# Kernel tuning notes

Measured on AMD Instinct MI355X. Metric: run time of the kernel, lower is better.

The kernel has to match this reference:

```python
import jax, jax.numpy as jnp
import numpy as np

B, NA, NB, DIM = 1024, 48, 24, 680  # batch, res_alpha(=res_gamma), res_beta, irreps dim = sum_{l<=7}(2l+1)^2


def setup_inputs() -> dict:
    key = jax.random.key(0)
    k1, k2, k3 = jax.random.split(key, 3)
    features = jax.random.normal(k1, (B, DIM), dtype=jnp.float32)
    D = jax.random.normal(k2, (NA, NB, NA, DIM), dtype=jnp.float32)  # stands in for the precomputed Wigner-D buffer
    qw = jax.random.uniform(k3, (NB,), dtype=jnp.float32)  # quadrature weights over beta
    return {"features": features, "D": D, "qw": qw}


def reference(features, D, qw):
    dim = D.shape[-1]
    scale = float(np.sqrt(dim))
    # to_grid: '...i,abci->...abc' / sqrt(dim)
    grid = jnp.einsum('ni,abci->nabc', features, D) / scale  # (B, na, nb, na)
    # from_grid: '...abc,abci,b->...i' * sqrt(dim)  (qw contracts the beta axis)
    out = jnp.einsum('nabc,abci,b->ni', grid, D, qw) * scale  # (B, dim)
    return out
```

## Files before the change

kernel.cpp:

```cpp
#include <hip/hip_runtime.h>
#include <stdint.h>

#define DIM    680
#define DPAD   768
#define NB_Q   24
#define SPLITS 72
#define STAGES 12
#define NTILE  6

typedef __bf16 bf16x8 __attribute__((ext_vector_type(8)));
typedef __bf16 bf16x2 __attribute__((ext_vector_type(2)));
typedef float  f32x16 __attribute__((ext_vector_type(16)));

typedef __attribute__((address_space(3))) unsigned       lds_u32;
typedef __attribute__((address_space(1))) const unsigned glb_u32;

__constant__ int c_tj[NTILE] = {0, 0, 0, 1, 1, 2};
__constant__ int c_ti[NTILE] = {0, 1, 2, 1, 2, 2};

static __device__ __forceinline__ unsigned f2bf(float x) {
    union { float f; unsigned u; } c; c.f = x;
    unsigned u = c.u;
    return (u + 0x7FFFu + ((u >> 16) & 1u)) >> 16;
}

static __device__ __forceinline__ unsigned pk2(float lo, float hi) {
    bf16x2 v = {(__bf16)lo, (__bf16)hi};
    return __builtin_bit_cast(unsigned, v);
}

static __device__ __forceinline__ float bf2f(unsigned short h) {
    union { unsigned u; float f; } c; c.u = ((unsigned)h) << 16;
    return c.f;
}

__global__ __launch_bounds__(512) void k12_gram(
        const float* __restrict__ D, const float* __restrict__ qw,
        uint2* __restrict__ parts) {
    __shared__ float sq[NB_Q];
    __shared__ uint4 smA[2048];
    __shared__ uint4 smB[2048];
    const int t  = threadIdx.x;
    const int h       = blockIdx.x;
    const int logical = (h & 7) * 54 + (h >> 3);
    const int split   = logical / 6;
    const int t6      = logical % 6;
    const int tj    = c_tj[t6];
    const int ti    = c_ti[t6];
    const bool diag = (tj == ti);
    const int cl_ = t & 255;
    const int hg  = t >> 8;
    const int cA  = tj * 256 + cl_;
    const int cB  = ti * 256 + cl_;
    const bool vA = (cA < DIM);
    const bool vB = (cB < DIM);
    const int cAc = vA ? cA : (DIM - 1);
    const int cBc = vB ? cB : (DIM - 1);
    const int wave  = t >> 6;
    const int lane  = t & 63;
    const int wm    = wave & 3;
    const int wn    = wave >> 2;
    const int cl    = lane & 31;
    const int half  = lane >> 5;

    f32x16 acc[2][4];
    const f32x16 zero = {};
#pragma unroll
    for (int a = 0; a < 2; ++a)
#pragma unroll
        for (int b = 0; b < 4; ++b) acc[a][b] = zero;

    float ra[32], rb[32];

#define K12_LOAD(reg_, st_, csrc_)                                            \
    do {                                                                      \
        const int g0_ = (split * STAGES + (st_)) * 64 + hg * 32;              \
        _Pragma("unroll")                                                     \
        for (int u_ = 0; u_ < 32; ++u_)                                       \
            reg_[u_] = D[(size_t)(g0_ + u_) * DIM + (csrc_)];                 \
    } while (0)

#define K12_CONV(reg_, valid_, sm_, st_)                                      \
    do {                                                                      \
        const int gg_ = (split * STAGES + (st_)) * 64 + hg * 32;              \
        _Pragma("unroll")                                                     \
        for (int kcg_ = 0; kcg_ < 4; ++kcg_) {                                \
            const int G_ = gg_ + kcg_ * 8;                                    \
            const int q_ = G_ / 48;                                           \
            const int r_ = G_ - q_ * 48;                                      \
            const float s0_ = sq[q_ % 24];                                    \
            const float s1_ = sq[(q_ + 1) % 24];                              \
            float e_[8];                                                      \
            _Pragma("unroll")                                                 \
            for (int j_ = 0; j_ < 8; ++j_) {                                  \
                const float sc_ = (r_ + j_ < 48) ? s0_ : s1_;                 \
                e_[j_] = (valid_) ? reg_[kcg_ * 8 + j_] * sc_ : 0.f;          \
            }                                                                 \
            uint4 o_;                                                         \
            o_.x = pk2(e_[0], e_[1]);                                         \
            o_.y = pk2(e_[2], e_[3]);                                         \
            o_.z = pk2(e_[4], e_[5]);                                         \
            o_.w = pk2(e_[6], e_[7]);                                         \
            sm_[cl_ * 8 + ((hg * 4 + kcg_) ^ (cl_ & 7))] = o_;                \
        }                                                                     \
    } while (0)

    K12_LOAD(ra, 0, cAc);
    if (!diag) K12_LOAD(rb, 0, cBc);
    if (t < NB_Q) sq[t] = sqrtf(qw[t]);
    asm volatile("s_waitcnt lgkmcnt(0)" ::: "memory");
    __builtin_amdgcn_s_barrier();

    for (int st = 0; st < STAGES; ++st) {
        K12_CONV(ra, vA, smA, st);
        if (st + 1 < STAGES) K12_LOAD(ra, st + 1, cAc);
        if (!diag) {
            K12_CONV(rb, vB, smB, st);
            if (st + 1 < STAGES) K12_LOAD(rb, st + 1, cBc);
        }
        asm volatile("s_waitcnt lgkmcnt(0)" ::: "memory");
        __builtin_amdgcn_s_barrier();

        const bf16x8* pA = reinterpret_cast<const bf16x8*>(smA);
        const bf16x8* pB = diag ? pA : reinterpret_cast<const bf16x8*>(smB);
#pragma unroll
        for (int t4 = 0; t4 < 4; ++t4) {
            const int kc = 2 * t4 + half;
            bf16x8 af[2], bfr[4];
#pragma unroll
            for (int ms = 0; ms < 2; ++ms) {
                const int col = wm * 64 + ms * 32 + cl;
                af[ms] = pA[col * 8 + (kc ^ (col & 7))];
            }
#pragma unroll
            for (int ns = 0; ns < 4; ++ns) {
                const int col = wn * 128 + ns * 32 + cl;
                bfr[ns] = pB[col * 8 + (kc ^ (col & 7))];
            }
            __builtin_amdgcn_s_setprio(1);
#pragma unroll
            for (int ms = 0; ms < 2; ++ms)
#pragma unroll
                for (int ns = 0; ns < 4; ++ns)
                    acc[ms][ns] = __builtin_amdgcn_mfma_f32_32x32x16_bf16(
                        af[ms], bfr[ns], acc[ms][ns], 0, 0, 0);
            __builtin_amdgcn_s_setprio(0);
        }
        asm volatile("s_waitcnt lgkmcnt(0)" ::: "memory");
        __builtin_amdgcn_s_barrier();
    }
#undef K12_LOAD
#undef K12_CONV

    uint2* pt = parts + (size_t)(split * NTILE + t6) * 16384;
#pragma unroll
    for (int ms = 0; ms < 2; ++ms) {
        const int rowb = wm * 64 + ms * 32 + 4 * half;
#pragma unroll
        for (int ns = 0; ns < 4; ++ns) {
            const int colt = wn * 128 + ns * 32 + cl;
#pragma unroll
            for (int q = 0; q < 4; ++q) {
                uint2 w;
                w.x = f2bf(acc[ms][ns][q * 4 + 0]) | (f2bf(acc[ms][ns][q * 4 + 1]) << 16);
                w.y = f2bf(acc[ms][ns][q * 4 + 2]) | (f2bf(acc[ms][ns][q * 4 + 3]) << 16);
                pt[(size_t)(((rowb >> 2) + 2 * q) * 256 + colt)] = w;
            }
        }
    }
}

__global__ __launch_bounds__(256) void kf_conv(const float* __restrict__ F,
                                               uint4* __restrict__ Fb) {
    const int idx = blockIdx.x * 256 + threadIdx.x;
    const int row = idx / 96;
    const int c0  = (idx % 96) * 8;
    uint4 o = {0u, 0u, 0u, 0u};
    if (c0 < DIM) {
        const float4 a = *reinterpret_cast<const float4*>(F + (size_t)row * DIM + c0);
        const float4 b = *reinterpret_cast<const float4*>(F + (size_t)row * DIM + c0 + 4);
        o.x = f2bf(a.x) | (f2bf(a.y) << 16);
        o.y = f2bf(a.z) | (f2bf(a.w) << 16);
        o.z = f2bf(b.x) | (f2bf(b.y) << 16);
        o.w = f2bf(b.z) | (f2bf(b.w) << 16);
    }
    Fb[idx] = o;
}

__global__ __launch_bounds__(256) void k2_reduce(
        const uint2* __restrict__ parts, unsigned short* __restrict__ Mb) {
    const int t6 = blockIdx.y;
    const int tj = c_tj[t6];
    const int ti = c_ti[t6];
    const int idx4 = blockIdx.x * 256 + threadIdx.x;
    const int w0 = idx4 * 2;
    const int quad = w0 >> 8;
    const int c = w0 & 255;
    float s[8] = {0.f, 0.f, 0.f, 0.f, 0.f, 0.f, 0.f, 0.f};
    const uint4* base = reinterpret_cast<const uint4*>(parts) + idx4;
#pragma unroll 8
    for (int sp = 0; sp < SPLITS; ++sp) {
        const uint4 u = base[(size_t)(sp * NTILE + t6) * 8192];
        s[0] += bf2f((unsigned short)(u.x & 0xFFFF));
        s[1] += bf2f((unsigned short)(u.x >> 16));
        s[2] += bf2f((unsigned short)(u.y & 0xFFFF));
        s[3] += bf2f((unsigned short)(u.y >> 16));
        s[4] += bf2f((unsigned short)(u.z & 0xFFFF));
        s[5] += bf2f((unsigned short)(u.z >> 16));
        s[6] += bf2f((unsigned short)(u.w & 0xFFFF));
        s[7] += bf2f((unsigned short)(u.w >> 16));
    }
    const int R = tj * 256 + 4 * quad;
    const int C = ti * 256 + c;
#pragma unroll
    for (int i = 0; i < 4; ++i) {
        const unsigned w = f2bf(s[i]) | (f2bf(s[4 + i]) << 16);
        *reinterpret_cast<unsigned*>(Mb + (size_t)(R + i) * DPAD + C) = w;
    }
    if (ti != tj) {
        uint2 m0, m1;
        m0.x = f2bf(s[0]) | (f2bf(s[1]) << 16);
        m0.y = f2bf(s[2]) | (f2bf(s[3]) << 16);
        m1.x = f2bf(s[4]) | (f2bf(s[5]) << 16);
        m1.y = f2bf(s[6]) | (f2bf(s[7]) << 16);
        *reinterpret_cast<uint2*>(Mb + (size_t)(C + 0) * DPAD + R) = m0;
        *reinterpret_cast<uint2*>(Mb + (size_t)(C + 1) * DPAD + R) = m1;
    }
}

__global__ __launch_bounds__(64) void k3_mfma(const uint4* __restrict__ Fb,
                                              const uint4* __restrict__ Mb,
                                              float* __restrict__ out) {
    __shared__ uint4 sA[2][512];
    __shared__ uint4 sB[2][512];
    const int t    = threadIdx.x;
    const int n0   = blockIdx.x * 64;
    const int i0   = blockIdx.y * 64;
    const int cl   = t & 31;
    const int half = t >> 5;

    f32x16 acc[2][2];
    const f32x16 zero = {};
    acc[0][0] = zero; acc[0][1] = zero; acc[1][0] = zero; acc[1][1] = zero;

#define K3_STAGE(ck_, buf_)                                                   \
    do {                                                                      \
        const int kcs_ = t & 7;                                               \
        _Pragma("unroll")                                                     \
        for (int j = 0; j < 8; ++j) {                                         \
            const int nl_ = j * 8 + (t >> 3);                                 \
            const int sc_ = (ck_) * 8 + (kcs_ ^ (nl_ & 7));                   \
            __builtin_amdgcn_global_load_lds(                                 \
                (glb_u32*)(Fb + (size_t)(n0 + nl_) * 96 + sc_),               \
                (lds_u32*)(&sA[(buf_)][j * 64 + t]), 16, 0, 0);               \
            __builtin_amdgcn_global_load_lds(                                 \
                (glb_u32*)(Mb + (size_t)(i0 + nl_) * 96 + sc_),               \
                (lds_u32*)(&sB[(buf_)][j * 64 + t]), 16, 0, 0);               \
        }                                                                     \
    } while (0)

    K3_STAGE(0, 0);
    asm volatile("s_waitcnt vmcnt(0)" ::: "memory");

    for (int ck = 0; ck < 12; ++ck) {
        const int cur = ck & 1;
        if (ck + 1 < 12) {
            asm volatile("s_waitcnt lgkmcnt(0)" ::: "memory");
            K3_STAGE(ck + 1, cur ^ 1);
            asm volatile("s_waitcnt vmcnt(16)" ::: "memory");
        }
        const bf16x8* pA = reinterpret_cast<const bf16x8*>(sA[cur]);
        const bf16x8* pB = reinterpret_cast<const bf16x8*>(sB[cur]);
#pragma unroll
        for (int t4 = 0; t4 < 4; ++t4) {
            const int kc = 2 * t4 + half;
            bf16x8 af[2], bv[2];
#pragma unroll
            for (int ms = 0; ms < 2; ++ms) {
                const int col = ms * 32 + cl;
                af[ms] = pA[col * 8 + (kc ^ (col & 7))];
            }
#pragma unroll
            for (int ns = 0; ns < 2; ++ns) {
                const int col = ns * 32 + cl;
                bv[ns] = pB[col * 8 + (kc ^ (col & 7))];
            }
#pragma unroll
            for (int ms = 0; ms < 2; ++ms)
#pragma unroll
                for (int ns = 0; ns < 2; ++ns)
                    acc[ms][ns] = __builtin_amdgcn_mfma_f32_32x32x16_bf16(
                        af[ms], bv[ns], acc[ms][ns], 0, 0, 0);
        }
    }
#undef K3_STAGE

#pragma unroll
    for (int ms = 0; ms < 2; ++ms) {
        const int rowb = ms * 32 + 4 * half;
#pragma unroll
        for (int ns = 0; ns < 2; ++ns) {
            const int col = i0 + ns * 32 + cl;
            if (col < DIM) {
#pragma unroll
                for (int q = 0; q < 4; ++q)
#pragma unroll
                    for (int j = 0; j < 4; ++j)
                        out[(size_t)(n0 + rowb + 8 * q + j) * DIM + col]
                            = acc[ms][ns][4 * q + j];
            }
        }
    }
}

extern "C" void kernel_launch(void* const* d_in, const int* in_sizes, int n_in,
                              void* d_out, int out_size, void* d_ws, size_t ws_size,
                              hipStream_t stream) {
    const float* F  = (const float*)d_in[0];
    const float* D  = (const float*)d_in[1];
    const float* qw = (const float*)d_in[2];
    float* out = (float*)d_out;
    char*  ws  = (char*)d_ws;

    uint2* parts = (uint2*)ws;
    const size_t parts_bytes = (size_t)SPLITS * NTILE * 16384 * 8;
    unsigned short* Mb = (unsigned short*)(ws + parts_bytes);
    const size_t mb_bytes = (size_t)DPAD * DPAD * 2;
    uint4* Fb = (uint4*)(ws + parts_bytes + mb_bytes);

    k12_gram<<<dim3(SPLITS * NTILE), 512, 0, stream>>>(D, qw, parts);
    kf_conv<<<dim3(1024 * DPAD / 8 / 256), 256, 0, stream>>>(F, Fb);
    k2_reduce<<<dim3(32, NTILE), 256, 0, stream>>>(parts, Mb);
    k3_mfma<<<dim3(16, 11), 64, 0, stream>>>(Fb, (const uint4*)Mb, out);
}
```

Measured before the change: 304.2 us.

## Double-buffer LDS tiles and vectorize global loads in gram kernel

The gram kernel now keeps two LDS buffers per operand, so conversion and storing of the next stage overlap with the MFMA work on the current one. This removes one barrier per stage. Global loads switch from 32 scalar column loads per thread to 8 float4 loads covering 4 adjacent columns. The LDS layout changes from a swizzled column-major scheme to a k-chunk-major layout. The change doubles LDS use, and the new unswizzled layout may bring bank conflicts. With only one barrier per stage, the buffer being written while another wave still reads it could race.

```diff
diff --git a/kernel.cpp b/kernel.cpp
--- a/kernel.cpp
+++ b/kernel.cpp
@@ -11,6 +11,7 @@
 typedef __bf16 bf16x8 __attribute__((ext_vector_type(8)));
 typedef __bf16 bf16x2 __attribute__((ext_vector_type(2)));
 typedef float  f32x16 __attribute__((ext_vector_type(16)));
+typedef float  f32x4  __attribute__((ext_vector_type(4)));
 
 typedef __attribute__((address_space(3))) unsigned       lds_u32;
 typedef __attribute__((address_space(1))) const unsigned glb_u32;
@@ -38,8 +39,8 @@
         const float* __restrict__ D, const float* __restrict__ qw,
         uint2* __restrict__ parts) {
     __shared__ float sq[NB_Q];
-    __shared__ uint4 smA[2048];
-    __shared__ uint4 smB[2048];
+    __shared__ uint4 smA[2][2048];
+    __shared__ uint4 smB[2][2048];
     const int t  = threadIdx.x;
     const int h       = blockIdx.x;
     const int logical = (h & 7) * 54 + (h >> 3);
@@ -48,14 +49,14 @@
     const int tj    = c_tj[t6];
     const int ti    = c_ti[t6];
     const bool diag = (tj == ti);
-    const int cl_ = t & 255;
-    const int hg  = t >> 8;
-    const int cA  = tj * 256 + cl_;
-    const int cB  = ti * 256 + cl_;
+    const int rg = t >> 6;
+    const int c0 = 4 * (t & 63);
+    const int cA = tj * 256 + c0;
+    const int cB = ti * 256 + c0;
     const bool vA = (cA < DIM);
     const bool vB = (cB < DIM);
-    const int cAc = vA ? cA : (DIM - 1);
-    const int cBc = vB ? cB : (DIM - 1);
+    const int cAc = vA ? cA : (DIM - 4);
+    const int cBc = vB ? cB : (DIM - 4);
     const int wave  = t >> 6;
     const int lane  = t & 63;
     const int wm    = wave & 3;
@@ -70,59 +71,67 @@
 #pragma unroll
         for (int b = 0; b < 4; ++b) acc[a][b] = zero;
 
-    float ra[32], rb[32];
+    f32x4 fa[8], fb[8];
 
 #define K12_LOAD(reg_, st_, csrc_)                                            \
     do {                                                                      \
-        const int g0_ = (split * STAGES + (st_)) * 64 + hg * 32;              \
+        const int g0_ = (split * STAGES + (st_)) * 64 + rg * 8;               \
         _Pragma("unroll")                                                     \
-        for (int u_ = 0; u_ < 32; ++u_)                                       \
-            reg_[u_] = D[(size_t)(g0_ + u_) * DIM + (csrc_)];                 \
+        for (int j_ = 0; j_ < 8; ++j_)                                        \
+            reg_[j_] = *reinterpret_cast<const f32x4*>(                       \
+                D + (size_t)(g0_ + j_) * DIM + (csrc_));                      \
     } while (0)
 
-#define K12_CONV(reg_, valid_, sm_, st_)                                      \
+#define K12_CONV(reg_, valid_, smx_, st_)                                     \
     do {                                                                      \
-        const int gg_ = (split * STAGES + (st_)) * 64 + hg * 32;              \
+        const int G_ = (split * STAGES + (st_)) * 64 + rg * 8;                \
+        const int q_ = G_ / 48;                                               \
+        const int r_ = G_ - q_ * 48;                                          \
+        const float s0_ = sq[q_ % 24];                                        \
+        const float s1_ = sq[(q_ + 1) % 24];                                  \
+        float sc_[8];                                                         \
         _Pragma("unroll")                                                     \
-        for (int kcg_ = 0; kcg_ < 4; ++kcg_) {                                \
-            const int G_ = gg_ + kcg_ * 8;                                    \
-            const int q_ = G_ / 48;                                           \
-            const int r_ = G_ - q_ * 48;                                      \
-            const float s0_ = sq[q_ % 24];                                    \
-            const float s1_ = sq[(q_ + 1) % 24];                              \
+        for (int j_ = 0; j_ < 8; ++j_) sc_[j_] = (r_ + j_ < 48) ? s0_ : s1_;  \
+        _Pragma("unroll")                                                     \
+        for (int jc_ = 0; jc_ < 4; ++jc_) {                                   \
             float e_[8];                                                      \
             _Pragma("unroll")                                                 \
-            for (int j_ = 0; j_ < 8; ++j_) {                                  \
-                const float sc_ = (r_ + j_ < 48) ? s0_ : s1_;                 \
-                e_[j_] = (valid_) ? reg_[kcg_ * 8 + j_] * sc_ : 0.f;          \
-            }                                                                 \
+            for (int j_ = 0; j_ < 8; ++j_)                                    \
+                e_[j_] = (valid_) ? reg_[j_][jc_] * sc_[j_] : 0.f;            \
             uint4 o_;                                                         \
             o_.x = pk2(e_[0], e_[1]);                                         \
             o_.y = pk2(e_[2], e_[3]);                                         \
             o_.z = pk2(e_[4], e_[5]);                                         \
             o_.w = pk2(e_[6], e_[7]);                                         \
-            sm_[cl_ * 8 + ((hg * 4 + kcg_) ^ (cl_ & 7))] = o_;                \
+            smx_[rg * 256 + c0 + jc_] = o_;          \
         }                                                                     \
     } while (0)
 
-    K12_LOAD(ra, 0, cAc);
-    if (!diag) K12_LOAD(rb, 0, cBc);
+    K12_LOAD(fa, 0, cAc);
+    if (!diag) K12_LOAD(fb, 0, cBc);
     if (t < NB_Q) sq[t] = sqrtf(qw[t]);
     asm volatile("s_waitcnt lgkmcnt(0)" ::: "memory");
     __builtin_amdgcn_s_barrier();
+    K12_CONV(fa, vA, smA[0], 0);
+    if (!diag) K12_CONV(fb, vB, smB[0], 0);
+    K12_LOAD(fa, 1, cAc);
+    if (!diag) K12_LOAD(fb, 1, cBc);
+    asm volatile("s_waitcnt lgkmcnt(0)" ::: "memory");
+    __builtin_amdgcn_s_barrier();
 
     for (int st = 0; st < STAGES; ++st) {
-        K12_CONV(ra, vA, smA, st);
-        if (st + 1 < STAGES) K12_LOAD(ra, st + 1, cAc);
-        if (!diag) {
-            K12_CONV(rb, vB, smB, st);
-            if (st + 1 < STAGES) K12_LOAD(rb, st + 1, cBc);
-        }
-        asm volatile("s_waitcnt lgkmcnt(0)" ::: "memory");
-        __builtin_amdgcn_s_barrier();
-
-        const bf16x8* pA = reinterpret_cast<const bf16x8*>(smA);
-        const bf16x8* pB = diag ? pA : reinterpret_cast<const bf16x8*>(smB);
+        const int cur = st & 1;
+        if (st + 1 < STAGES) {
+            K12_CONV(fa, vA, smA[cur ^ 1], st + 1);
+            if (st + 2 < STAGES) K12_LOAD(fa, st + 2, cAc);
+            if (!diag) {
+                K12_CONV(fb, vB, smB[cur ^ 1], st + 1);
+                if (st + 2 < STAGES) K12_LOAD(fb, st + 2, cBc);
+            }
+        }
+
+        const bf16x8* pA = reinterpret_cast<const bf16x8*>(smA[cur]);
+        const bf16x8* pB = diag ? pA : reinterpret_cast<const bf16x8*>(smB[cur]);
 #pragma unroll
         for (int t4 = 0; t4 < 4; ++t4) {
             const int kc = 2 * t4 + half;
@@ -130,12 +139,12 @@
 #pragma unroll
             for (int ms = 0; ms < 2; ++ms) {
                 const int col = wm * 64 + ms * 32 + cl;
-                af[ms] = pA[col * 8 + (kc ^ (col & 7))];
+                af[ms] = pA[kc * 256 + col];
             }
 #pragma unroll
             for (int ns = 0; ns < 4; ++ns) {
                 const int col = wn * 128 + ns * 32 + cl;
-                bfr[ns] = pB[col * 8 + (kc ^ (col & 7))];
+                bfr[ns] = pB[kc * 256 + col];
             }
             __builtin_amdgcn_s_setprio(1);
 #pragma unroll
```

Result: faster. 277.3 us (-8.8%).
